# Kernel tuning notes

Measured on AMD Instinct MI355X. Metric: run time of the kernel, lower is better.

The kernel has to match this reference:

```python
import jax, jax.numpy as jnp
import numpy as np

D_MODEL = 1024
NUM_HEADS = 16
D_K = D_MODEL // NUM_HEADS
B, S = 2, 2048


def setup_inputs() -> dict:
    key = jax.random.key(0)
    ks = jax.random.split(key, 11)
    sc = 1.0 / np.sqrt(D_MODEL)
    return {
        "query": jax.random.normal(ks[0], (B, S, D_MODEL), jnp.float32),
        "key": jax.random.normal(ks[1], (B, S, D_MODEL), jnp.float32),
        "value": jax.random.normal(ks[2], (B, S, D_MODEL), jnp.float32),
        "Wq": jax.random.normal(ks[3], (D_MODEL, D_MODEL), jnp.float32) * sc,
        "bq": jnp.zeros((D_MODEL,), jnp.float32),
        "Wk": jax.random.normal(ks[4], (D_MODEL, D_MODEL), jnp.float32) * sc,
        "bk": jnp.zeros((D_MODEL,), jnp.float32),
        "Wv": jax.random.normal(ks[5], (D_MODEL, D_MODEL), jnp.float32) * sc,
        "bv": jnp.zeros((D_MODEL,), jnp.float32),
        "Wo": jax.random.normal(ks[6], (D_MODEL, D_MODEL), jnp.float32) * sc,
        "bo": jnp.zeros((D_MODEL,), jnp.float32),
    }


def reference(query, key, value, Wq, bq, Wk, bk, Wv, bv, Wo, bo):
    b, sq, _ = query.shape
    # projections -> [B, H, S, d_k]
    def split_heads(x):
        return x.reshape(b, -1, NUM_HEADS, D_K).transpose(0, 2, 1, 3)

    q = split_heads(query @ Wq + bq)
    k = split_heads(key @ Wk + bk)
    v = split_heads(value @ Wv + bv)

    scores = jnp.einsum("bhqd,bhkd->bhqk", q, k) / np.sqrt(D_K).astype(np.float32)
    probs = jax.nn.softmax(scores, axis=-1)  # dropout p=0 (eval) -> identity
    attn = jnp.einsum("bhqk,bhkd->bhqd", probs, v)
    attn = attn.transpose(0, 2, 1, 3).reshape(b, sq, D_MODEL)
    out = attn @ Wo + bo
    return out, probs
```

## Files before the change

kernel.cpp:

```cpp
#include <hip/hip_runtime.h>


typedef __bf16 bf16x8 __attribute__((ext_vector_type(8)));
typedef float f32x4 __attribute__((ext_vector_type(4)));

typedef const unsigned int __attribute__((address_space(1))) as1c_uint;
typedef unsigned int __attribute__((address_space(3))) as3_uint;

#define S_LEN 2048
#define DM 1024
#define NH 16
#define DK 64
#define BATCH 2
#define M_ROWS 4096
#define KE 0.18033688f

__device__ __forceinline__ unsigned short f2bfu(float f) {
  union { __bf16 b; unsigned short u; } cv;
  cv.b = (__bf16)f;
  return cv.u;
}

__device__ __forceinline__ float bfu2f(unsigned short u) {
  union { float f; unsigned int i; } c;
  c.i = ((unsigned int)u) << 16;
  return c.f;
}

__device__ __forceinline__ void gload_lds16(const void* g, void* l) {
  __builtin_amdgcn_global_load_lds((as1c_uint*)g, (as3_uint*)l, 16, 0, 0);
}

__global__ __launch_bounds__(256) void cvt3_kernel(
    const float* __restrict__ q, const float* __restrict__ k,
    const float* __restrict__ v, unsigned short* __restrict__ oq,
    unsigned short* __restrict__ ok_, unsigned short* __restrict__ ov) {
  const float* in = blockIdx.z == 0 ? q : (blockIdx.z == 1 ? k : v);
  unsigned short* out = blockIdx.z == 0 ? oq : (blockIdx.z == 1 ? ok_ : ov);
  size_t i = (size_t)blockIdx.x * 256 + threadIdx.x;
  float4 f = ((const float4*)in)[i];
  ushort4 u;
  u.x = f2bfu(f.x); u.y = f2bfu(f.y); u.z = f2bfu(f.z); u.w = f2bfu(f.w);
  ((ushort4*)out)[i] = u;
}

__global__ __launch_bounds__(256) void wtrans_kernel(
    const float* __restrict__ w0, const float* __restrict__ w1,
    const float* __restrict__ w2, const float* __restrict__ w3,
    unsigned short* __restrict__ o0, unsigned short* __restrict__ o1,
    unsigned short* __restrict__ o2, unsigned short* __restrict__ o3) {
  const float* W = blockIdx.z == 0 ? w0 : (blockIdx.z == 1 ? w1 : (blockIdx.z == 2 ? w2 : w3));
  unsigned short* WT = blockIdx.z == 0 ? o0 : (blockIdx.z == 1 ? o1 : (blockIdx.z == 2 ? o2 : o3));
  __shared__ float tile[32][33];
  int tx = threadIdx.x & 31, ty = threadIdx.x >> 5;
  int bx = blockIdx.x * 32, by = blockIdx.y * 32;
#pragma unroll
  for (int i = 0; i < 32; i += 8)
    tile[ty + i][tx] = W[(size_t)(by + ty + i) * DM + bx + tx];
  __syncthreads();
#pragma unroll
  for (int i = 0; i < 32; i += 8)
    WT[(size_t)(bx + ty + i) * DM + by + tx] = f2bfu(tile[tx][ty + i]);
}

template <int EPI>
__device__ __forceinline__ void gemm_core(const unsigned short* __restrict__ A,
                                          const unsigned short* __restrict__ BT,
                                          const float* __restrict__ bias,
                                          void* __restrict__ C) {
  __shared__ __attribute__((aligned(16))) unsigned short As[3][128 * 32];
  __shared__ __attribute__((aligned(16))) unsigned short Bs[3][128 * 32];
  const int tid = threadIdx.x;
  const int w = tid >> 6, l = tid & 63;
  const int wr = w >> 1, wc = w & 1;
  const int fr = l & 15, fq = l >> 4;
  const int bid = blockIdx.y * 8 + blockIdx.x;
  const int swz = (bid & 7) * 32 + (bid >> 3);
  const int n0 = (swz & 7) * 128, m0 = (swz >> 3) * 128;
  const int srow = l >> 2;
  const int sk8 = (l & 3) * 8;
  f32x4 acc[4][4] = {};

#define GSTAGE(itn, buf)                                                      \
  {                                                                           \
    _Pragma("unroll") for (int c = 0; c < 2; c++) {                           \
      int rr = c * 64 + w * 16;                                               \
      gload_lds16(A + (size_t)(m0 + rr + srow) * DM + (itn) * 32 + sk8,       \
                  &As[buf][rr * 32]);                                         \
      gload_lds16(BT + (size_t)(n0 + rr + srow) * DM + (itn) * 32 + sk8,      \
                  &Bs[buf][rr * 32]);                                         \
    }                                                                         \
  }

  const int KIT = DM / 32;
  GSTAGE(0, 0);
  GSTAGE(1, 1);
  asm volatile("s_waitcnt vmcnt(4)" : : : "memory");
  __builtin_amdgcn_s_barrier();
  for (int it = 0; it < KIT; ++it) {
    const int cur = it % 3;
    if (it + 2 < KIT) GSTAGE(it + 2, (it + 2) % 3);
    bf16x8 af[4], bfv[4];
#pragma unroll
    for (int m = 0; m < 4; m++)
      af[m] = *(const bf16x8*)&As[cur][(wr * 64 + m * 16 + fr) * 32 + fq * 8];
#pragma unroll
    for (int n = 0; n < 4; n++)
      bfv[n] = *(const bf16x8*)&Bs[cur][(wc * 64 + n * 16 + fr) * 32 + fq * 8];
#pragma unroll
    for (int m = 0; m < 4; m++)
#pragma unroll
      for (int n = 0; n < 4; n++)
        acc[m][n] = __builtin_amdgcn_mfma_f32_16x16x32_bf16(af[m], bfv[n], acc[m][n], 0, 0, 0);
    if (it + 1 < KIT) {
      if (it + 2 < KIT) {
        asm volatile("s_waitcnt vmcnt(4)" : : : "memory");
      } else {
        asm volatile("s_waitcnt vmcnt(0)" : : : "memory");
      }
      __builtin_amdgcn_s_barrier();
    }
  }
#undef GSTAGE

#pragma unroll
  for (int m = 0; m < 4; m++) {
#pragma unroll
    for (int n = 0; n < 4; n++) {
      const int col = n0 + wc * 64 + n * 16 + fr;
      const float bv = bias[col];
#pragma unroll
      for (int j = 0; j < 4; j++) {
        const int row = m0 + wr * 64 + m * 16 + fq * 4 + j;
        const float v = acc[m][n][j] + bv;
        if (EPI == 0) {
          ((float*)C)[(size_t)row * DM + col] = v;
        } else {
          const int b = row >> 11, s = row & (S_LEN - 1);
          const int h = col >> 6, d = col & (DK - 1);
          ((unsigned short*)C)[(((size_t)b * NH + h) * S_LEN + s) * DK + d] = f2bfu(v);
        }
      }
    }
  }
}

__global__ __launch_bounds__(256) void gemm_qkv_kernel(
    const unsigned short* __restrict__ xq, const unsigned short* __restrict__ xk,
    const unsigned short* __restrict__ xv, const unsigned short* __restrict__ wq,
    const unsigned short* __restrict__ wk, const unsigned short* __restrict__ wv,
    const float* __restrict__ bq, const float* __restrict__ bk,
    const float* __restrict__ bv, unsigned short* __restrict__ oq,
    unsigned short* __restrict__ okk, unsigned short* __restrict__ ov) {
  const int z = blockIdx.z;
  const unsigned short* A = z == 0 ? xq : (z == 1 ? xk : xv);
  const unsigned short* BT = z == 0 ? wq : (z == 1 ? wk : wv);
  const float* bias = z == 0 ? bq : (z == 1 ? bk : bv);
  unsigned short* C = z == 0 ? oq : (z == 1 ? okk : ov);
  gemm_core<1>(A, BT, bias, C);
}

__global__ __launch_bounds__(256) void gemm_out_kernel(
    const unsigned short* __restrict__ A, const unsigned short* __restrict__ BT,
    const float* __restrict__ bias, float* __restrict__ C) {
  gemm_core<0>(A, BT, bias, C);
}

__global__ __launch_bounds__(256) void vtrans_kernel(
    const unsigned short* __restrict__ V, unsigned short* __restrict__ VT) {
  __shared__ __attribute__((aligned(16))) unsigned short t[64][72];
  const int bh = blockIdx.y, s0 = blockIdx.x * 64;
  const unsigned short* v = V + ((size_t)bh * S_LEN + s0) * DK;
  const int tid = threadIdx.x;
#pragma unroll
  for (int i = 0; i < 4; i++) {
    int idx = tid + 256 * i;
    int r = idx >> 4, c4 = (idx & 15) * 4;
    *(ushort4*)&t[r][c4] = *(const ushort4*)(v + (size_t)r * DK + c4);
  }
  __syncthreads();
  unsigned short* o = VT + (size_t)bh * DK * S_LEN + s0;
#pragma unroll
  for (int i = 0; i < 4; i++) {
    int idx = tid + 256 * i;
    int d = idx >> 4, s4 = (idx & 15) * 4;
    ushort4 u;
    u.x = t[s4 + 0][d]; u.y = t[s4 + 1][d];
    u.z = t[s4 + 2][d]; u.w = t[s4 + 3][d];
    *(ushort4*)(o + (size_t)d * S_LEN + s4) = u;
  }
}

__global__ __launch_bounds__(256, 4) void attn_kernel(
    const unsigned short* __restrict__ Qp, const unsigned short* __restrict__ Kp,
    const unsigned short* __restrict__ VT, float* __restrict__ probs,
    unsigned short* __restrict__ attnc) {
  const int flat = blockIdx.y * 32 + blockIdx.x;
  const int xcd = flat & 7, r = flat >> 3;
  const int bh = xcd * 4 + (r >> 5);
  const int tile = r & 31;
  const int w = threadIdx.x >> 6, l = threadIdx.x & 63;
  const int fr = l & 15, fq = l >> 4;
  const int q0 = tile * 64 + w * 16;
  const int qrow = q0 + fr;
  const unsigned short* Qh = Qp + (size_t)bh * S_LEN * DK;
  const unsigned short* Kh = Kp + (size_t)bh * S_LEN * DK;
  const unsigned short* Vh = VT + (size_t)bh * DK * S_LEN;
  float* ph = probs + (size_t)bh * S_LEN * S_LEN;

  __shared__ __attribute__((aligned(16))) unsigned short Sb[4][64 * 64];
  __shared__ __attribute__((aligned(16))) unsigned short Pfb[4][16][64];

  const int srow8 = l >> 3;
  const int sgran = ((l & 7) ^ (l >> 3)) << 3;
  const int kr7 = fr & 7;

  bf16x8 qf[2];
  qf[0] = *(const bf16x8*)(Qh + (size_t)qrow * DK + fq * 8);
  qf[1] = *(const bf16x8*)(Qh + (size_t)qrow * DK + 32 + fq * 8);

  const int NIT = S_LEN / 64;

#define STAGE_P1(itn, buf)                                                    \
  {                                                                           \
    _Pragma("unroll") for (int i = 0; i < 2; i++)                             \
        gload_lds16(Kh + (size_t)((itn) * 64 + w * 16 + i * 8 + srow8) * DK + \
                        sgran,                                                \
                    &Sb[buf][(w * 16 + i * 8) * 64]);                         \
  }

  float ps4[4] = {0.f, 0.f, 0.f, 0.f};
  STAGE_P1(0, 0);
  STAGE_P1(1, 1);
  asm volatile("s_waitcnt vmcnt(2)" : : : "memory");
  __builtin_amdgcn_s_barrier();
  for (int it = 0; it < NIT; ++it) {
    const unsigned short* kcur = &Sb[it % 3][0];
    if (it + 2 < NIT) STAGE_P1(it + 2, (it + 2) % 3);
#pragma unroll
    for (int t = 0; t < 4; t++) {
      const int rk = t * 16 + fr;
      const bf16x8 a0 = *(const bf16x8*)&kcur[rk * 64 + ((fq ^ kr7) << 3)];
      const bf16x8 a1 = *(const bf16x8*)&kcur[rk * 64 + (((fq + 4) ^ kr7) << 3)];
      f32x4 s4 = {0.f, 0.f, 0.f, 0.f};
      s4 = __builtin_amdgcn_mfma_f32_16x16x32_bf16(a0, qf[0], s4, 0, 0, 0);
      s4 = __builtin_amdgcn_mfma_f32_16x16x32_bf16(a1, qf[1], s4, 0, 0, 0);
#pragma unroll
      for (int j = 0; j < 4; j++) ps4[j] += __builtin_amdgcn_exp2f(s4[j] * KE);
    }
    if (it + 1 < NIT) {
      if (it + 2 < NIT) {
        asm volatile("s_waitcnt vmcnt(2)" : : : "memory");
      } else {
        asm volatile("s_waitcnt vmcnt(0)" : : : "memory");
      }
      __builtin_amdgcn_s_barrier();
    }
  }
#undef STAGE_P1
  float psum = (ps4[0] + ps4[1]) + (ps4[2] + ps4[3]);
  psum += __shfl_xor(psum, 16, 64);
  psum += __shfl_xor(psum, 32, 64);
  const float pinv = 1.f / psum;
  __builtin_amdgcn_s_barrier();

  f32x4 oacc[4] = {};
  const int strow = l >> 4;
  const int stc16 = l & 15;
#pragma unroll
  for (int i = 0; i < 2; i++) {
    gload_lds16(Kh + (size_t)(w * 16 + i * 8 + srow8) * DK + sgran,
                &Sb[0][(w * 16 + i * 8) * 64]);
    gload_lds16(Vh + (size_t)(w * 16 + i * 8 + srow8) * S_LEN + sgran,
                &Sb[2][(w * 16 + i * 8) * 64]);
  }
  asm volatile("s_waitcnt vmcnt(0)" : : : "memory");
  __builtin_amdgcn_s_barrier();
  for (int it = 0; it < NIT; ++it) {
    const int cur = it & 1;
    const int skb = it * 64;
    if (it + 1 < NIT) {
#pragma unroll
      for (int i = 0; i < 2; i++) {
        gload_lds16(Kh + (size_t)(skb + 64 + w * 16 + i * 8 + srow8) * DK + sgran,
                    &Sb[cur ^ 1][(w * 16 + i * 8) * 64]);
        gload_lds16(Vh + (size_t)(w * 16 + i * 8 + srow8) * S_LEN + (skb + 64) + sgran,
                    &Sb[2 + (cur ^ 1)][(w * 16 + i * 8) * 64]);
      }
    }
    if (it > 0) {
      const int skbp = skb - 64;
#pragma unroll
      for (int i = 0; i < 4; i++) {
        const int row = 4 * i + strow;
        const int g2 = ((stc16 >> 1) ^ (row & 7));
        const ushort4 pb4 = *(const ushort4*)&Pfb[w][row][g2 * 8 + (l & 1) * 4];
        f32x4 pv4;
        pv4[0] = bfu2f(pb4.x); pv4[1] = bfu2f(pb4.y);
        pv4[2] = bfu2f(pb4.z); pv4[3] = bfu2f(pb4.w);
        __builtin_nontemporal_store(
            pv4, (f32x4*)(ph + (size_t)(q0 + row) * S_LEN + skbp + stc16 * 4));
      }
    }
#pragma unroll
    for (int sub = 0; sub < 2; sub++) {
#pragma unroll
      for (int t = 0; t < 2; t++) {
        const int rk = sub * 32 + t * 16 + fr;
        const bf16x8 a0 = *(const bf16x8*)&Sb[cur][rk * 64 + ((fq ^ kr7) << 3)];
        const bf16x8 a1 = *(const bf16x8*)&Sb[cur][rk * 64 + (((fq + 4) ^ kr7) << 3)];
        f32x4 s4 = {0.f, 0.f, 0.f, 0.f};
        s4 = __builtin_amdgcn_mfma_f32_16x16x32_bf16(a0, qf[0], s4, 0, 0, 0);
        s4 = __builtin_amdgcn_mfma_f32_16x16x32_bf16(a1, qf[1], s4, 0, 0, 0);
        ushort4 pb;
#pragma unroll
        for (int j = 0; j < 4; j++)
          ((unsigned short*)&pb)[j] = f2bfu(__builtin_amdgcn_exp2f(s4[j] * KE) * pinv);
        const int g = (sub * 4 + t * 2 + (fq >> 1)) ^ kr7;
        *(ushort4*)&Pfb[w][fr][g * 8 + (fq & 1) * 4] = pb;
      }
      const int gr = (sub * 4 + fq) ^ kr7;
      const bf16x8 pa = *(const bf16x8*)&Pfb[w][fr][gr * 8];
      __builtin_amdgcn_s_setprio(1);
#pragma unroll
      for (int n = 0; n < 4; n++) {
        const bf16x8 vf =
            *(const bf16x8*)&Sb[2 + cur][(n * 16 + fr) * 64 + (((sub * 4 + fq) ^ kr7) << 3)];
        oacc[n] = __builtin_amdgcn_mfma_f32_16x16x32_bf16(pa, vf, oacc[n], 0, 0, 0);
      }
      __builtin_amdgcn_s_setprio(0);
    }
    if (it + 1 < NIT) {
      if (it == 0) {
        asm volatile("s_waitcnt vmcnt(0)" : : : "memory");
      } else {
        asm volatile("s_waitcnt vmcnt(4)" : : : "memory");
      }
      __builtin_amdgcn_s_barrier();
    }
  }
  {
    const int skbp = (NIT - 1) * 64;
#pragma unroll
    for (int i = 0; i < 4; i++) {
      const int row = 4 * i + strow;
      const int g2 = ((stc16 >> 1) ^ (row & 7));
      const ushort4 pb4 = *(const ushort4*)&Pfb[w][row][g2 * 8 + (l & 1) * 4];
      f32x4 pv4;
      pv4[0] = bfu2f(pb4.x); pv4[1] = bfu2f(pb4.y);
      pv4[2] = bfu2f(pb4.z); pv4[3] = bfu2f(pb4.w);
      __builtin_nontemporal_store(
          pv4, (f32x4*)(ph + (size_t)(q0 + row) * S_LEN + skbp + stc16 * 4));
    }
  }

  const int b = bh >> 4, h = bh & (NH - 1);
#pragma unroll
  for (int n = 0; n < 4; n++) {
#pragma unroll
    for (int j = 0; j < 4; j++) {
      const int row = q0 + fq * 4 + j, col = h * DK + n * 16 + fr;
      attnc[(size_t)((size_t)b * S_LEN + row) * DM + col] = f2bfu(oacc[n][j]);
    }
  }
}

extern "C" void kernel_launch(void* const* d_in, const int* in_sizes, int n_in,
                              void* d_out, int out_size, void* d_ws, size_t ws_size,
                              hipStream_t stream) {
  const float* query = (const float*)d_in[0];
  const float* key   = (const float*)d_in[1];
  const float* value = (const float*)d_in[2];
  const float* Wq = (const float*)d_in[3];
  const float* bq = (const float*)d_in[4];
  const float* Wk = (const float*)d_in[5];
  const float* bk = (const float*)d_in[6];
  const float* Wv = (const float*)d_in[7];
  const float* bv = (const float*)d_in[8];
  const float* Wo = (const float*)d_in[9];
  const float* bo = (const float*)d_in[10];

  char* ws = (char*)d_ws;
  const size_t XSZ = (size_t)M_ROWS * DM * 2;
  const size_t WSZ = (size_t)DM * DM * 2;
  unsigned short* xq  = (unsigned short*)(ws);
  unsigned short* xk  = (unsigned short*)(ws + XSZ);
  unsigned short* xv  = (unsigned short*)(ws + 2 * XSZ);
  unsigned short* wtq = (unsigned short*)(ws + 3 * XSZ);
  unsigned short* wtk = (unsigned short*)(ws + 3 * XSZ + WSZ);
  unsigned short* wtv = (unsigned short*)(ws + 3 * XSZ + 2 * WSZ);
  unsigned short* wto = (unsigned short*)(ws + 3 * XSZ + 3 * WSZ);
  unsigned short* qp  = (unsigned short*)(ws + 3 * XSZ + 4 * WSZ);
  unsigned short* kp  = (unsigned short*)(ws + 4 * XSZ + 4 * WSZ);
  unsigned short* vp  = (unsigned short*)(ws + 5 * XSZ + 4 * WSZ);
  unsigned short* vT    = xk;
  unsigned short* attnc = xq;

  float* out = (float*)d_out;
  float* probs = (float*)d_out + (size_t)BATCH * S_LEN * DM;

  cvt3_kernel<<<dim3(4096, 1, 3), 256, 0, stream>>>(query, key, value, xq, xk, xv);
  wtrans_kernel<<<dim3(32, 32, 4), 256, 0, stream>>>(Wq, Wk, Wv, Wo, wtq, wtk, wtv, wto);
  gemm_qkv_kernel<<<dim3(8, 32, 3), 256, 0, stream>>>(xq, xk, xv, wtq, wtk, wtv,
                                                      bq, bk, bv, qp, kp, vp);
  vtrans_kernel<<<dim3(32, 32), 256, 0, stream>>>(vp, vT);
  attn_kernel<<<dim3(32, 32), 256, 0, stream>>>(qp, kp, vT, probs, attnc);
  gemm_out_kernel<<<dim3(8, 32), 256, 0, stream>>>(attnc, wto, bo, out);
}
```

Measured before the change: 230.3 us.

## Double attention block to 8 waves covering 128 query rows

```diff
diff --git a/kernel.cpp b/kernel.cpp
--- a/kernel.cpp
+++ b/kernel.cpp
@@ -191,17 +191,17 @@
   }
 }
 
-__global__ __launch_bounds__(256, 4) void attn_kernel(
+__global__ __launch_bounds__(512, 6) void attn_kernel(
     const unsigned short* __restrict__ Qp, const unsigned short* __restrict__ Kp,
     const unsigned short* __restrict__ VT, float* __restrict__ probs,
     unsigned short* __restrict__ attnc) {
-  const int flat = blockIdx.y * 32 + blockIdx.x;
+  const int flat = blockIdx.y * 16 + blockIdx.x;
   const int xcd = flat & 7, r = flat >> 3;
-  const int bh = xcd * 4 + (r >> 5);
-  const int tile = r & 31;
+  const int bh = xcd * 4 + (r >> 4);
+  const int tile = r & 15;
   const int w = threadIdx.x >> 6, l = threadIdx.x & 63;
   const int fr = l & 15, fq = l >> 4;
-  const int q0 = tile * 64 + w * 16;
+  const int q0 = tile * 128 + w * 16;
   const int qrow = q0 + fr;
   const unsigned short* Qh = Qp + (size_t)bh * S_LEN * DK;
   const unsigned short* Kh = Kp + (size_t)bh * S_LEN * DK;
@@ -209,7 +209,7 @@
   float* ph = probs + (size_t)bh * S_LEN * S_LEN;
 
   __shared__ __attribute__((aligned(16))) unsigned short Sb[4][64 * 64];
-  __shared__ __attribute__((aligned(16))) unsigned short Pfb[4][16][64];
+  __shared__ __attribute__((aligned(16))) unsigned short Pfb[8][16][64];
 
   const int srow8 = l >> 3;
   const int sgran = ((l & 7) ^ (l >> 3)) << 3;
@@ -222,17 +222,18 @@
   const int NIT = S_LEN / 64;
 
 #define STAGE_P1(itn, buf)                                                    \
-  {                                                                           \
-    _Pragma("unroll") for (int i = 0; i < 2; i++)                             \
-        gload_lds16(Kh + (size_t)((itn) * 64 + w * 16 + i * 8 + srow8) * DK + \
-                        sgran,                                                \
-                    &Sb[buf][(w * 16 + i * 8) * 64]);                         \
-  }
+  gload_lds16(Kh + (size_t)((itn) * 64 + w * 8 + srow8) * DK + sgran,         \
+              &Sb[buf][(w * 8 + srow8 - srow8) * 64 + (w * 8) * 64]);         \
+
+#undef STAGE_P1
+#define STAGE_P1(itn, buf)                                                    \
+  gload_lds16(Kh + (size_t)((itn) * 64 + w * 8 + srow8) * DK + sgran,         \
+              &Sb[buf][(w * 8) * 64]);
 
   float ps4[4] = {0.f, 0.f, 0.f, 0.f};
   STAGE_P1(0, 0);
   STAGE_P1(1, 1);
-  asm volatile("s_waitcnt vmcnt(2)" : : : "memory");
+  asm volatile("s_waitcnt vmcnt(1)" : : : "memory");
   __builtin_amdgcn_s_barrier();
   for (int it = 0; it < NIT; ++it) {
     const unsigned short* kcur = &Sb[it % 3][0];
@@ -250,7 +251,7 @@
     }
     if (it + 1 < NIT) {
       if (it + 2 < NIT) {
-        asm volatile("s_waitcnt vmcnt(2)" : : : "memory");
+        asm volatile("s_waitcnt vmcnt(1)" : : : "memory");
       } else {
         asm volatile("s_waitcnt vmcnt(0)" : : : "memory");
       }
@@ -267,26 +268,18 @@
   f32x4 oacc[4] = {};
   const int strow = l >> 4;
   const int stc16 = l & 15;
-#pragma unroll
-  for (int i = 0; i < 2; i++) {
-    gload_lds16(Kh + (size_t)(w * 16 + i * 8 + srow8) * DK + sgran,
-                &Sb[0][(w * 16 + i * 8) * 64]);
-    gload_lds16(Vh + (size_t)(w * 16 + i * 8 + srow8) * S_LEN + sgran,
-                &Sb[2][(w * 16 + i * 8) * 64]);
-  }
+  gload_lds16(Kh + (size_t)(w * 8 + srow8) * DK + sgran, &Sb[0][(w * 8) * 64]);
+  gload_lds16(Vh + (size_t)(w * 8 + srow8) * S_LEN + sgran, &Sb[2][(w * 8) * 64]);
   asm volatile("s_waitcnt vmcnt(0)" : : : "memory");
   __builtin_amdgcn_s_barrier();
   for (int it = 0; it < NIT; ++it) {
     const int cur = it & 1;
     const int skb = it * 64;
     if (it + 1 < NIT) {
-#pragma unroll
-      for (int i = 0; i < 2; i++) {
-        gload_lds16(Kh + (size_t)(skb + 64 + w * 16 + i * 8 + srow8) * DK + sgran,
-                    &Sb[cur ^ 1][(w * 16 + i * 8) * 64]);
-        gload_lds16(Vh + (size_t)(w * 16 + i * 8 + srow8) * S_LEN + (skb + 64) + sgran,
-                    &Sb[2 + (cur ^ 1)][(w * 16 + i * 8) * 64]);
-      }
+      gload_lds16(Kh + (size_t)(skb + 64 + w * 8 + srow8) * DK + sgran,
+                  &Sb[cur ^ 1][(w * 8) * 64]);
+      gload_lds16(Vh + (size_t)(w * 8 + srow8) * S_LEN + (skb + 64) + sgran,
+                  &Sb[2 + (cur ^ 1)][(w * 8) * 64]);
     }
     if (it > 0) {
       const int skbp = skb - 64;
@@ -404,6 +397,6 @@
   gemm_qkv_kernel<<<dim3(8, 32, 3), 256, 0, stream>>>(xq, xk, xv, wtq, wtk, wtv,
                                                       bq, bk, bv, qp, kp, vp);
   vtrans_kernel<<<dim3(32, 32), 256, 0, stream>>>(vp, vT);
-  attn_kernel<<<dim3(32, 32), 256, 0, stream>>>(qp, kp, vT, probs, attnc);
+  attn_kernel<<<dim3(16, 32), 512, 0, stream>>>(qp, kp, vT, probs, attnc);
   gemm_out_kernel<<<dim3(8, 32), 256, 0, stream>>>(attnc, wto, bo, out);
 }
```

After: 242.9 us. +5.4%, slower.
